# Optimization experiments

Measured on AMD Instinct MI355X. Metric: run time of the kernel, lower is better.

## Reference

```python
import jax, jax.numpy as jnp
import numpy as np

B, C, H, W = 32, 1024, 32, 32  # N = H*W must equal C for the attn_c * attn_s broadcast
C8 = C // 8


def setup_inputs() -> dict:
    key = jax.random.key(0)
    ks = jax.random.split(key, 9)
    s = 1.0 / np.sqrt(C)
    return {
        "z": jax.random.normal(ks[0], (B, C, H, W), jnp.float32),
        "x": jax.random.normal(ks[1], (B, C, H, W), jnp.float32),
        "y": jax.random.normal(ks[2], (B, C, H, W), jnp.float32),
        "Wq": jax.random.normal(ks[3], (C8, C), jnp.float32) * s,
        "bq": jax.random.normal(ks[4], (C8,), jnp.float32) * 0.01,
        "Wk": jax.random.normal(ks[5], (C8, C), jnp.float32) * s,
        "bk": jax.random.normal(ks[6], (C8,), jnp.float32) * 0.01,
        "Wv": jax.random.normal(ks[7], (C, C), jnp.float32) * s,
        "bv": jax.random.normal(ks[8], (C,), jnp.float32) * 0.01,
    }


def reference(z, x, y, Wq, bq, Wk, bk, Wv, bv):
    b, c, h, w = x.shape
    n = h * w
    xf = x.reshape(b, c, n)
    yf = y.reshape(b, c, n)
    zf = z.reshape(b, c, n)

    # 1x1 convs == channel matmuls
    q = jnp.einsum('oc,bcn->bon', Wq, xf) + bq[None, :, None]   # (B, C/8, N)
    k = jnp.einsum('oc,bcn->bon', Wk, yf) + bk[None, :, None]   # (B, C/8, N)

    # channel-projected spatial attention: (B, N, N)
    energy_c = jnp.einsum('bcn,bcm->bnm', q, k)
    attention_c = jax.nn.softmax(energy_c, axis=-1)

    # raw channel attention: (B, C, C)
    energy_s = jnp.einsum('bcn,bdn->bcd', xf, yf)
    energy_s = jnp.max(energy_s, axis=-1, keepdims=True) - energy_s
    attention_s = jax.nn.softmax(energy_s, axis=-1)

    # multiplicative combine + third softmax (requires N == C)
    attention = jax.nn.softmax(attention_c * attention_s, axis=-1)

    v = jnp.einsum('oc,bcn->bon', Wv, zf) + bv[None, :, None]   # (B, C, N)
    # out[b,c,m] = sum_n v[b,c,n] * attention[b,m,n]  (value @ attention^T)
    out = jnp.einsum('bcn,bmn->bcm', v, attention)
    return z + out.reshape(b, c, h, w)
```

## Files before the change

kernel.cpp:

```cpp
#include <hip/hip_runtime.h>
#include <hip/hip_bf16.h>

typedef __attribute__((ext_vector_type(8))) short s8_t;
typedef __attribute__((ext_vector_type(4))) float f4_t;

__device__ __forceinline__ unsigned short f2bf(float f) {
  union { float f; unsigned u; } x; x.f = f;
  unsigned r = x.u + 0x7fffu + ((x.u >> 16) & 1u);
  return (unsigned short)(r >> 16);
}

__device__ __forceinline__ void split2(float e0, float e1, unsigned& hp, unsigned& lp) {
  unsigned b0 = __float_as_uint(e0), b1 = __float_as_uint(e1);
  unsigned h0 = b0 & 0xFFFF0000u, h1 = b1 & 0xFFFF0000u;
  hp = (b0 >> 16) | h1;
  float l0 = e0 - __uint_as_float(h0), l1 = e1 - __uint_as_float(h1);
  lp = (__float_as_uint(l0) >> 16) | (__float_as_uint(l1) & 0xFFFF0000u);
}

__device__ __forceinline__ void gload16(const void* g, void* l) {
  __builtin_amdgcn_global_load_lds(
      (const __attribute__((address_space(1))) void*)g,
      (__attribute__((address_space(3))) void*)l, 16, 0, 0);
}

__device__ __forceinline__ void swz_grid(int& bx, int& by, int& bz) {
  const int gx = gridDim.x, gy = gridDim.y;
  const int nwg = gx * gy * gridDim.z;
  const int flat = (blockIdx.z * gy + blockIdx.y) * gx + blockIdx.x;
  const int s = (flat & 7) * (nwg >> 3) + (flat >> 3);
  bx = s % gx;
  const int r = s / gx;
  by = r % gy;
  bz = r / gy;
}

__global__ __launch_bounds__(256) void k_convert(const float* __restrict__ in,
                                                 unsigned short* __restrict__ out, int n) {
  int i = (blockIdx.x * 256 + threadIdx.x) * 8;
  if (i >= n) return;
  float4 a = *(const float4*)(in + i);
  float4 b = *(const float4*)(in + i + 4);
  ushort4 u0; u0.x = f2bf(a.x); u0.y = f2bf(a.y); u0.z = f2bf(a.z); u0.w = f2bf(a.w);
  ushort4 u1; u1.x = f2bf(b.x); u1.y = f2bf(b.y); u1.z = f2bf(b.z); u1.w = f2bf(b.w);
  *(ushort4*)(out + i) = u0;
  *(ushort4*)(out + i + 4) = u1;
}

__global__ __launch_bounds__(256) void k_transp32(const float* __restrict__ in,
                                                  float* __restrict__ out) {
  __shared__ float tile[64][65];
  const int t = threadIdx.x, b = blockIdx.z;
  const int r0 = blockIdx.y * 64, c0 = blockIdx.x * 64;
  const float* ip = in + (size_t)b * 1048576;
  float* op = out + (size_t)b * 1048576;
  const int tr = t >> 4, tc = (t & 15) * 4;
#pragma unroll
  for (int p = 0; p < 4; ++p) {
    int r = p * 16 + tr;
    float4 v = *(const float4*)(ip + (size_t)(r0 + r) * 1024 + c0 + tc);
    tile[r][tc] = v.x; tile[r][tc + 1] = v.y; tile[r][tc + 2] = v.z; tile[r][tc + 3] = v.w;
  }
  __syncthreads();
#pragma unroll
  for (int p = 0; p < 4; ++p) {
    int n = p * 16 + tr;
    float4 w;
    w.x = tile[tc][n]; w.y = tile[tc + 1][n]; w.z = tile[tc + 2][n]; w.w = tile[tc + 3][n];
    *(float4*)(op + (size_t)(c0 + n) * 1024 + r0 + tc) = w;
  }
}

__global__ __launch_bounds__(256) void k_transpbf(const float* __restrict__ in,
                                                  unsigned short* __restrict__ outt) {
  __shared__ unsigned short tile[64][72];
  const int t = threadIdx.x, b = blockIdx.z;
  const int r0 = blockIdx.y * 64, c0 = blockIdx.x * 64;
  const float* ip = in + (size_t)b * 1048576;
  const int tr = t >> 4, tc = (t & 15) * 4;
#pragma unroll
  for (int p = 0; p < 4; ++p) {
    int r = p * 16 + tr;
    float4 v = *(const float4*)(ip + (size_t)(r0 + r) * 1024 + c0 + tc);
    tile[r][tc] = f2bf(v.x); tile[r][tc + 1] = f2bf(v.y);
    tile[r][tc + 2] = f2bf(v.z); tile[r][tc + 3] = f2bf(v.w);
  }
  __syncthreads();
#pragma unroll
  for (int p = 0; p < 4; ++p) {
    int n = p * 16 + tr;
    ushort4 w;
    w.x = tile[tc][n]; w.y = tile[tc + 1][n]; w.z = tile[tc + 2][n]; w.w = tile[tc + 3][n];
    *(ushort4*)(outt + (size_t)b * 1048576 + (size_t)(c0 + n) * 1024 + r0 + tc) = w;
  }
}

__device__ __forceinline__ void split_write(unsigned short* buf, int wbase,
                                            const float* av, const float* bv) {
  unsigned ah[8], al[8], bh[8], bl[8];
#pragma unroll
  for (int p = 0; p < 8; ++p) {
    split2(av[2 * p], av[2 * p + 1], ah[p], al[p]);
    split2(bv[2 * p], bv[2 * p + 1], bh[p], bl[p]);
  }
  *(uint4*)(buf + wbase) = *(uint4*)(ah);
  *(uint4*)(buf + wbase + 8) = *(uint4*)(ah + 4);
  *(uint4*)(buf + 4096 + wbase) = *(uint4*)(al);
  *(uint4*)(buf + 4096 + wbase + 8) = *(uint4*)(al + 4);
  *(uint4*)(buf + 8192 + wbase) = *(uint4*)(bh);
  *(uint4*)(buf + 8192 + wbase + 8) = *(uint4*)(bh + 4);
  *(uint4*)(buf + 12288 + wbase) = *(uint4*)(bl);
  *(uint4*)(buf + 12288 + wbase + 8) = *(uint4*)(bl + 4);
}

template <int BIAS_MODE>
__global__ __launch_bounds__(256) void k_mfma3(
    const float* __restrict__ A, int lda, long long sA,
    const float* __restrict__ B, int ldb, long long sB,
    float* __restrict__ C, int ldc, long long sC,
    const float* __restrict__ bias, int K) {
  __shared__ __align__(16) unsigned short sm[16384];
  int bxs, bys, bz; swz_grid(bxs, bys, bz);
  const int tid = threadIdx.x;
  const int lane = tid & 63, wave = tid >> 6;
  const int wr = wave >> 1, wc = wave & 1;
  const int m0 = bxs * 128, n0 = bys * 128;

  const int sr = tid >> 1, sh = (tid & 1) * 16;
  const float* ag = A + (long long)bz * sA + (long long)(m0 + sr) * lda + sh;
  const float* bg = B + (long long)bz * sB + (long long)(n0 + sr) * ldb + sh;
  const int wbase = sr * 32 + sh;

  const int lr = lane & 15, lg = lane >> 4;
  const int fa = (wr * 64 + lr) * 32 + lg * 8;
  const int fb = (wc * 64 + lr) * 32 + lg * 8;

  f4_t acc[4][4];
#pragma unroll
  for (int i = 0; i < 4; ++i)
#pragma unroll
    for (int j = 0; j < 4; ++j) acc[i][j] = (f4_t)0.f;

  for (int k0 = 0; k0 < K; k0 += 32) {
    float av[16], bv[16];
#pragma unroll
    for (int p = 0; p < 4; ++p) {
      *(float4*)(av + p * 4) = *(const float4*)(ag + p * 4);
      *(float4*)(bv + p * 4) = *(const float4*)(bg + p * 4);
    }
    split_write(sm, wbase, av, bv);
    ag += 32; bg += 32;
    __syncthreads();
    const unsigned short* Ahp = sm;
    const unsigned short* Alp = sm + 4096;
    const unsigned short* Bhp = sm + 8192;
    const unsigned short* Blp = sm + 12288;
    s8_t fah[4], fbh[4], ftmp[4];
#pragma unroll
    for (int f = 0; f < 4; ++f) {
      fah[f] = *(const s8_t*)(Ahp + fa + f * 512);
      fbh[f] = *(const s8_t*)(Bhp + fb + f * 512);
    }
#pragma unroll
    for (int i = 0; i < 4; ++i)
#pragma unroll
      for (int j = 0; j < 4; ++j)
        acc[i][j] = __builtin_amdgcn_mfma_f32_16x16x32_bf16(fah[i], fbh[j], acc[i][j], 0, 0, 0);
#pragma unroll
    for (int f = 0; f < 4; ++f) ftmp[f] = *(const s8_t*)(Blp + fb + f * 512);
#pragma unroll
    for (int i = 0; i < 4; ++i)
#pragma unroll
      for (int j = 0; j < 4; ++j)
        acc[i][j] = __builtin_amdgcn_mfma_f32_16x16x32_bf16(fah[i], ftmp[j], acc[i][j], 0, 0, 0);
#pragma unroll
    for (int f = 0; f < 4; ++f) ftmp[f] = *(const s8_t*)(Alp + fa + f * 512);
#pragma unroll
    for (int i = 0; i < 4; ++i)
#pragma unroll
      for (int j = 0; j < 4; ++j)
        acc[i][j] = __builtin_amdgcn_mfma_f32_16x16x32_bf16(ftmp[i], fbh[j], acc[i][j], 0, 0, 0);
    __syncthreads();
  }

#pragma unroll
  for (int i = 0; i < 4; ++i) {
    const int rbase = m0 + wr * 64 + i * 16 + lg * 4;
#pragma unroll
    for (int j = 0; j < 4; ++j) {
      const int col = n0 + wc * 64 + j * 16 + lr;
      float bc = (BIAS_MODE == 2) ? bias[col] : 0.f;
#pragma unroll
      for (int e = 0; e < 4; ++e) {
        float v = acc[i][j][e];
        if (BIAS_MODE == 2) v += bc;
        C[(long long)bz * sC + (long long)(rbase + e) * ldc + col] = v;
      }
    }
  }
}

template <int BIAS_MODE, bool OUT_BF16, bool RESID>
__global__ __launch_bounds__(256) void k_mfma(
    const unsigned short* __restrict__ A, int lda, long long sA,
    const unsigned short* __restrict__ B, int ldb, long long sB,
    void* __restrict__ Cp, int ldc, long long sC,
    const float* __restrict__ bias,
    const float* __restrict__ resid, long long sR, int K) {
  __shared__ __align__(16) unsigned short As[12288];
  __shared__ __align__(16) unsigned short Bs[12288];
  int bxs, bys, bz; swz_grid(bxs, bys, bz);
  const int tid = threadIdx.x;
  const int lane = tid & 63, wave = tid >> 6;
  const int wr = wave >> 1, wc = wave & 1;
  const int m0 = bxs * 128, n0 = bys * 128;

  const int ch0 = wave * 64 + lane, ch1 = ch0 + 256;
  const unsigned short* pa0 = A + (long long)bz * sA + (long long)(m0 + (ch0 >> 2)) * lda + (ch0 & 3) * 8;
  const unsigned short* pa1 = A + (long long)bz * sA + (long long)(m0 + (ch1 >> 2)) * lda + (ch1 & 3) * 8;
  const unsigned short* pb0 = B + (long long)bz * sB + (long long)(n0 + (ch0 >> 2)) * ldb + (ch0 & 3) * 8;
  const unsigned short* pb1 = B + (long long)bz * sB + (long long)(n0 + (ch1 >> 2)) * ldb + (ch1 & 3) * 8;

  const int lr = lane & 15, lg = lane >> 4;
  const int fa = (wr * 64 + lr) * 32 + lg * 8;
  const int fb = (wc * 64 + lr) * 32 + lg * 8;

  f4_t acc[4][4];
#pragma unroll
  for (int i = 0; i < 4; ++i)
#pragma unroll
    for (int j = 0; j < 4; ++j) acc[i][j] = (f4_t)0.f;

  char* a0 = (char*)As; char* a1 = a0 + 8192; char* a2 = a0 + 16384;
  char* b0 = (char*)Bs; char* b1 = b0 + 8192; char* b2 = b0 + 16384;

  auto stage = [&](char* la, char* lb) {
    gload16(pa0, la + wave * 1024);
    gload16(pa1, la + 4096 + wave * 1024);
    gload16(pb0, lb + wave * 1024);
    gload16(pb1, lb + 4096 + wave * 1024);
    pa0 += 32; pa1 += 32; pb0 += 32; pb1 += 32;
  };

  const int nt = K >> 5;
  stage(a0, b0);
  stage(a1, b1);

  for (int t = 0; t < nt; ++t) {
    if (t + 2 < nt) {
      stage(a2, b2);
      asm volatile("s_waitcnt vmcnt(8)" ::: "memory");
    } else if (t + 1 < nt) {
      asm volatile("s_waitcnt vmcnt(4)" ::: "memory");
    } else {
      asm volatile("s_waitcnt vmcnt(0)" ::: "memory");
    }
    __builtin_amdgcn_sched_barrier(0);
    __builtin_amdgcn_s_barrier();
    __builtin_amdgcn_sched_barrier(0);
    const unsigned short* ap = (const unsigned short*)a0;
    const unsigned short* bp = (const unsigned short*)b0;
    s8_t af[4], bf[4];
#pragma unroll
    for (int f = 0; f < 4; ++f) {
      af[f] = *(const s8_t*)(ap + fa + f * 512);
      bf[f] = *(const s8_t*)(bp + fb + f * 512);
    }
#pragma unroll
    for (int i = 0; i < 4; ++i)
#pragma unroll
      for (int j = 0; j < 4; ++j)
        acc[i][j] = __builtin_amdgcn_mfma_f32_16x16x32_bf16(af[i], bf[j], acc[i][j], 0, 0, 0);
    __builtin_amdgcn_sched_barrier(0);
    __builtin_amdgcn_s_barrier();
    __builtin_amdgcn_sched_barrier(0);
    char* ta = a0; a0 = a1; a1 = a2; a2 = ta;
    char* tb = b0; b0 = b1; b1 = b2; b2 = tb;
  }

#pragma unroll
  for (int i = 0; i < 4; ++i) {
    const int rbase = m0 + wr * 64 + i * 16 + lg * 4;
#pragma unroll
    for (int j = 0; j < 4; ++j) {
      const int col = n0 + wc * 64 + j * 16 + lr;
#pragma unroll
      for (int e = 0; e < 4; ++e) {
        const int row = rbase + e;
        float v = acc[i][j][e];
        if (BIAS_MODE == 1) v += bias[row];
        const long long off = (long long)bz * sC + (long long)row * ldc + col;
        if (RESID) v += resid[(long long)bz * sR + (long long)row * ldc + col];
        if (OUT_BF16) ((unsigned short*)Cp)[off] = f2bf(v);
        else          ((float*)Cp)[off] = v;
      }
    }
  }
}

__device__ __forceinline__ float wave_red_max(float v) {
#pragma unroll
  for (int o = 32; o > 0; o >>= 1) v = fmaxf(v, __shfl_down(v, o, 64));
  return v;
}
__device__ __forceinline__ float wave_red_sum(float v) {
#pragma unroll
  for (int o = 32; o > 0; o >>= 1) v += __shfl_down(v, o, 64);
  return v;
}
__device__ __forceinline__ float block_red_max(float v, float* red) {
  v = wave_red_max(v);
  if ((threadIdx.x & 63) == 0) red[threadIdx.x >> 6] = v;
  __syncthreads();
  v = fmaxf(fmaxf(red[0], red[1]), fmaxf(red[2], red[3]));
  __syncthreads();
  return v;
}
__device__ __forceinline__ float block_red_sum(float v, float* red) {
  v = wave_red_sum(v);
  if ((threadIdx.x & 63) == 0) red[threadIdx.x >> 6] = v;
  __syncthreads();
  v = red[0] + red[1] + red[2] + red[3];
  __syncthreads();
  return v;
}

__global__ __launch_bounds__(256) void k_combine(float* __restrict__ ec,
                                                 const float* __restrict__ es) {
  __shared__ float red[4];
  const size_t row = blockIdx.x;
  float* cp = ec + row * 1024;
  const float* sp = es + row * 1024;
  const int tid = threadIdx.x;
  float4 c4 = ((const float4*)cp)[tid];
  float4 s4 = ((const float4*)sp)[tid];

  float mx = fmaxf(fmaxf(c4.x, c4.y), fmaxf(c4.z, c4.w));
  mx = block_red_max(mx, red);
  float e0 = __expf(c4.x - mx), e1 = __expf(c4.y - mx);
  float e2 = __expf(c4.z - mx), e3 = __expf(c4.w - mx);
  float sc = block_red_sum(e0 + e1 + e2 + e3, red);

  float t0 = -s4.x, t1 = -s4.y, t2 = -s4.z, t3 = -s4.w;
  float mt = fmaxf(fmaxf(t0, t1), fmaxf(t2, t3));
  mt = block_red_max(mt, red);
  float f0 = __expf(t0 - mt), f1 = __expf(t1 - mt);
  float f2 = __expf(t2 - mt), f3 = __expf(t3 - mt);
  float ss = block_red_sum(f0 + f1 + f2 + f3, red);

  const float rc = 1.f / sc, rs = 1.f / ss;
  float g0 = __expf((e0 * rc) * (f0 * rs));
  float g1 = __expf((e1 * rc) * (f1 * rs));
  float g2 = __expf((e2 * rc) * (f2 * rs));
  float g3 = __expf((e3 * rc) * (f3 * rs));
  float s3 = block_red_sum(g0 + g1 + g2 + g3, red);
  const float r3 = 1.f / s3;
  ushort4 o;
  o.x = f2bf(g0 * r3); o.y = f2bf(g1 * r3); o.z = f2bf(g2 * r3); o.w = f2bf(g3 * r3);
  ((ushort4*)cp)[tid] = o;
}

extern "C" void kernel_launch(void* const* d_in, const int* in_sizes, int n_in,
                              void* d_out, int out_size, void* d_ws, size_t ws_size,
                              hipStream_t stream) {
  const float* z = (const float*)d_in[0];
  const float* x = (const float*)d_in[1];
  const float* y = (const float*)d_in[2];
  const float* Wq = (const float*)d_in[3];
  const float* bq = (const float*)d_in[4];
  const float* Wk = (const float*)d_in[5];
  const float* bk = (const float*)d_in[6];
  const float* Wv = (const float*)d_in[7];
  const float* bv = (const float*)d_in[8];
  float* out = (float*)d_out;

  char* ws = (char*)d_ws;
  float* es = (float*)ws;
  unsigned short* z_t = (unsigned short*)ws;
  unsigned short* v_bf = z_t + 33554432;
  char* wsB = ws + 134217728;
  float* xytf = (float*)wsB;
  float* ec = (float*)wsB;
  unsigned short* attn = (unsigned short*)wsB;
  char* wsC = ws + 268435456;
  float* q_t = (float*)wsC;
  float* k_t = q_t + 4194304;
  unsigned short* wv = (unsigned short*)wsC;

  dim3 blk(256);
  hipLaunchKernelGGL(k_transp32, dim3(16, 16, 32), blk, 0, stream, x, xytf);
  hipLaunchKernelGGL((k_mfma3<2>), dim3(8, 1, 32), blk, 0, stream,
                     xytf, 1024, 1048576LL, Wq, 1024, 0LL, q_t, 128, 131072LL, bq, 1024);
  hipLaunchKernelGGL(k_transp32, dim3(16, 16, 32), blk, 0, stream, y, xytf);
  hipLaunchKernelGGL((k_mfma3<2>), dim3(8, 1, 32), blk, 0, stream,
                     xytf, 1024, 1048576LL, Wk, 1024, 0LL, k_t, 128, 131072LL, bk, 1024);
  hipLaunchKernelGGL((k_mfma3<0>), dim3(8, 8, 32), blk, 0, stream,
                     x, 1024, 1048576LL, y, 1024, 1048576LL, es, 1024, 1048576LL,
                     (const float*)nullptr, 1024);
  hipLaunchKernelGGL((k_mfma3<0>), dim3(8, 8, 32), blk, 0, stream,
                     q_t, 128, 131072LL, k_t, 128, 131072LL, ec, 1024, 1048576LL,
                     (const float*)nullptr, 128);
  hipLaunchKernelGGL(k_combine, dim3(32768), blk, 0, stream, ec, es);
  hipLaunchKernelGGL(k_transpbf, dim3(16, 16, 32), blk, 0, stream, z, z_t);
  hipLaunchKernelGGL(k_convert, dim3(512), blk, 0, stream, Wv, wv, 1048576);
  hipLaunchKernelGGL((k_mfma<1, true, false>), dim3(8, 8, 32), blk, 0, stream,
                     wv, 1024, 0LL, z_t, 1024, 1048576LL, (void*)v_bf, 1024, 1048576LL,
                     bv, (const float*)nullptr, 0LL, 1024);
  hipLaunchKernelGGL((k_mfma<0, false, true>), dim3(8, 8, 32), blk, 0, stream,
                     v_bf, 1024, 1048576LL, attn, 2048, 2097152LL, (void*)out, 1024, 1048576LL,
                     (const float*)nullptr, z, 1048576LL, 1024);
}
```

Measured before the change: 866.2 us.

## Fuse Q/K projections into split-bf16 MFMA kernel and enlarge bf16 GEMM tiles

```diff
diff --git a/kernel.cpp b/kernel.cpp
--- a/kernel.cpp
+++ b/kernel.cpp
@@ -8,6 +8,14 @@
   union { float f; unsigned u; } x; x.f = f;
   unsigned r = x.u + 0x7fffu + ((x.u >> 16) & 1u);
   return (unsigned short)(r >> 16);
+}
+
+__device__ __forceinline__ void split1(float v, unsigned short& h, unsigned short& l) {
+  unsigned b = __float_as_uint(v);
+  unsigned hb = b & 0xFFFF0000u;
+  h = (unsigned short)(b >> 16);
+  float lo = v - __uint_as_float(hb);
+  l = (unsigned short)(__float_as_uint(lo) >> 16);
 }
 
 __device__ __forceinline__ void split2(float e0, float e1, unsigned& hp, unsigned& lp) {
@@ -47,13 +55,14 @@
   *(ushort4*)(out + i + 4) = u1;
 }
 
-__global__ __launch_bounds__(256) void k_transp32(const float* __restrict__ in,
-                                                  float* __restrict__ out) {
+__global__ __launch_bounds__(256) void k_tsplitT(const float* __restrict__ in,
+                                                 unsigned short* __restrict__ th,
+                                                 unsigned short* __restrict__ tl) {
   __shared__ float tile[64][65];
-  const int t = threadIdx.x, b = blockIdx.z;
+  const int t = threadIdx.x, bz = blockIdx.z;
   const int r0 = blockIdx.y * 64, c0 = blockIdx.x * 64;
-  const float* ip = in + (size_t)b * 1048576;
-  float* op = out + (size_t)b * 1048576;
+  const float* ip = in + (size_t)bz * 1048576;
+  const size_t ob = (size_t)bz * 1048576;
   const int tr = t >> 4, tc = (t & 15) * 4;
 #pragma unroll
   for (int p = 0; p < 4; ++p) {
@@ -65,9 +74,11 @@
 #pragma unroll
   for (int p = 0; p < 4; ++p) {
     int n = p * 16 + tr;
-    float4 w;
-    w.x = tile[tc][n]; w.y = tile[tc + 1][n]; w.z = tile[tc + 2][n]; w.w = tile[tc + 3][n];
-    *(float4*)(op + (size_t)(c0 + n) * 1024 + r0 + tc) = w;
+    float a = tile[tc][n], b = tile[tc + 1][n], c = tile[tc + 2][n], d = tile[tc + 3][n];
+    ushort4 h, l;
+    split1(a, h.x, l.x); split1(b, h.y, l.y); split1(c, h.z, l.z); split1(d, h.w, l.w);
+    *(ushort4*)(th + ob + (size_t)(c0 + n) * 1024 + r0 + tc) = h;
+    *(ushort4*)(tl + ob + (size_t)(c0 + n) * 1024 + r0 + tc) = l;
   }
 }
 
@@ -200,45 +211,144 @@
   }
 }
 
+__global__ __launch_bounds__(256) void k_qk3p(
+    const unsigned short* __restrict__ Axh, const unsigned short* __restrict__ Axl,
+    const unsigned short* __restrict__ Ayh, const unsigned short* __restrict__ Ayl,
+    const float* __restrict__ Wqf, const float* __restrict__ Wkf,
+    const float* __restrict__ bqf, const float* __restrict__ bkf,
+    float* __restrict__ Qt, float* __restrict__ Kt) {
+  __shared__ __align__(16) unsigned short smAh[4096], smAl[4096], smBh[4096], smBl[4096];
+  int bx, by, bz; swz_grid(bx, by, bz);
+  const unsigned short* Ah = by ? Ayh : Axh;
+  const unsigned short* Al = by ? Ayl : Axl;
+  const float* Bf = by ? Wkf : Wqf;
+  const float* bias = by ? bkf : bqf;
+  float* Of = by ? Kt : Qt;
+
+  const int tid = threadIdx.x, lane = tid & 63, wave = tid >> 6;
+  const int wr = wave >> 1, wc = wave & 1;
+  const int m0 = bx * 128;
+
+  const int ch0 = wave * 64 + lane, ch1 = ch0 + 256;
+  const int r0 = ch0 >> 2, kc0 = (ch0 & 3) * 8, r1 = ch1 >> 2, kc1 = (ch1 & 3) * 8;
+  const unsigned short* pah0 = Ah + (long long)bz * 1048576 + (long long)(m0 + r0) * 1024 + kc0;
+  const unsigned short* pah1 = Ah + (long long)bz * 1048576 + (long long)(m0 + r1) * 1024 + kc1;
+  const unsigned short* pal0 = Al + (long long)bz * 1048576 + (long long)(m0 + r0) * 1024 + kc0;
+  const unsigned short* pal1 = Al + (long long)bz * 1048576 + (long long)(m0 + r1) * 1024 + kc1;
+  char* dAh0 = (char*)smAh + wave * 1024; char* dAh1 = dAh0 + 4096;
+  char* dAl0 = (char*)smAl + wave * 1024; char* dAl1 = dAl0 + 4096;
+
+  const int sr = tid >> 1, sh = (tid & 1) * 16;
+  const float* bg = Bf + (long long)sr * 1024 + sh;
+  const int wbase = sr * 32 + sh;
+
+  const int lr = lane & 15, lg = lane >> 4;
+  const int fa = (wr * 64 + lr) * 32 + lg * 8;
+  const int fb = (wc * 64 + lr) * 32 + lg * 8;
+
+  f4_t acc[4][4];
+#pragma unroll
+  for (int i = 0; i < 4; ++i)
+#pragma unroll
+    for (int j = 0; j < 4; ++j) acc[i][j] = (f4_t)0.f;
+
+  for (int k0 = 0; k0 < 1024; k0 += 32) {
+    gload16(pah0, dAh0); gload16(pah1, dAh1);
+    gload16(pal0, dAl0); gload16(pal1, dAl1);
+    pah0 += 32; pah1 += 32; pal0 += 32; pal1 += 32;
+    float bv[16];
+#pragma unroll
+    for (int p = 0; p < 4; ++p) *(float4*)(bv + p * 4) = *(const float4*)(bg + p * 4);
+    bg += 32;
+    unsigned bh[8], bl[8];
+#pragma unroll
+    for (int p = 0; p < 8; ++p) split2(bv[2 * p], bv[2 * p + 1], bh[p], bl[p]);
+    *(uint4*)(smBh + wbase) = *(uint4*)(bh);
+    *(uint4*)(smBh + wbase + 8) = *(uint4*)(bh + 4);
+    *(uint4*)(smBl + wbase) = *(uint4*)(bl);
+    *(uint4*)(smBl + wbase + 8) = *(uint4*)(bl + 4);
+    __syncthreads();
+    s8_t fah[4], fbh[4], ft[4];
+#pragma unroll
+    for (int f = 0; f < 4; ++f) {
+      fah[f] = *(const s8_t*)(smAh + fa + f * 512);
+      fbh[f] = *(const s8_t*)(smBh + fb + f * 512);
+    }
+#pragma unroll
+    for (int i = 0; i < 4; ++i)
+#pragma unroll
+      for (int j = 0; j < 4; ++j)
+        acc[i][j] = __builtin_amdgcn_mfma_f32_16x16x32_bf16(fah[i], fbh[j], acc[i][j], 0, 0, 0);
+#pragma unroll
+    for (int f = 0; f < 4; ++f) ft[f] = *(const s8_t*)(smBl + fb + f * 512);
+#pragma unroll
+    for (int i = 0; i < 4; ++i)
+#pragma unroll
+      for (int j = 0; j < 4; ++j)
+        acc[i][j] = __builtin_amdgcn_mfma_f32_16x16x32_bf16(fah[i], ft[j], acc[i][j], 0, 0, 0);
+#pragma unroll
+    for (int f = 0; f < 4; ++f) ft[f] = *(const s8_t*)(smAl + fa + f * 512);
+#pragma unroll
+    for (int i = 0; i < 4; ++i)
+#pragma unroll
+      for (int j = 0; j < 4; ++j)
+        acc[i][j] = __builtin_amdgcn_mfma_f32_16x16x32_bf16(ft[i], fbh[j], acc[i][j], 0, 0, 0);
+    __syncthreads();
+  }
+
+#pragma unroll
+  for (int i = 0; i < 4; ++i) {
+    const int rbase = m0 + wr * 64 + i * 16 + lg * 4;
+#pragma unroll
+    for (int j = 0; j < 4; ++j) {
+      const int col = wc * 64 + j * 16 + lr;
+      const float bc = bias[col];
+#pragma unroll
+      for (int e = 0; e < 4; ++e)
+        Of[(long long)bz * 131072 + (long long)(rbase + e) * 128 + col] = acc[i][j][e] + bc;
+    }
+  }
+}
+
 template <int BIAS_MODE, bool OUT_BF16, bool RESID>
-__global__ __launch_bounds__(256) void k_mfma(
+__global__ __launch_bounds__(512) void k_mfma256(
     const unsigned short* __restrict__ A, int lda, long long sA,
     const unsigned short* __restrict__ B, int ldb, long long sB,
     void* __restrict__ Cp, int ldc, long long sC,
     const float* __restrict__ bias,
     const float* __restrict__ resid, long long sR, int K) {
-  __shared__ __align__(16) unsigned short As[12288];
-  __shared__ __align__(16) unsigned short Bs[12288];
+  __shared__ __align__(16) unsigned short As[24576];
+  __shared__ __align__(16) unsigned short Bs[24576];
   int bxs, bys, bz; swz_grid(bxs, bys, bz);
   const int tid = threadIdx.x;
   const int lane = tid & 63, wave = tid >> 6;
-  const int wr = wave >> 1, wc = wave & 1;
-  const int m0 = bxs * 128, n0 = bys * 128;
-
-  const int ch0 = wave * 64 + lane, ch1 = ch0 + 256;
-  const unsigned short* pa0 = A + (long long)bz * sA + (long long)(m0 + (ch0 >> 2)) * lda + (ch0 & 3) * 8;
-  const unsigned short* pa1 = A + (long long)bz * sA + (long long)(m0 + (ch1 >> 2)) * lda + (ch1 & 3) * 8;
-  const unsigned short* pb0 = B + (long long)bz * sB + (long long)(n0 + (ch0 >> 2)) * ldb + (ch0 & 3) * 8;
-  const unsigned short* pb1 = B + (long long)bz * sB + (long long)(n0 + (ch1 >> 2)) * ldb + (ch1 & 3) * 8;
+  const int wr = wave >> 2, wc = wave & 3;
+  const int m0 = bxs * 256, n0 = bys * 256;
+
+  const int cA0 = tid, cA1 = tid + 512;
+  const unsigned short* pa0 = A + (long long)bz * sA + (long long)(m0 + (cA0 >> 2)) * lda + (cA0 & 3) * 8;
+  const unsigned short* pa1 = A + (long long)bz * sA + (long long)(m0 + (cA1 >> 2)) * lda + (cA1 & 3) * 8;
+  const unsigned short* pb0 = B + (long long)bz * sB + (long long)(n0 + (cA0 >> 2)) * ldb + (cA0 & 3) * 8;
+  const unsigned short* pb1 = B + (long long)bz * sB + (long long)(n0 + (cA1 >> 2)) * ldb + (cA1 & 3) * 8;
 
   const int lr = lane & 15, lg = lane >> 4;
-  const int fa = (wr * 64 + lr) * 32 + lg * 8;
+  const int fa = (wr * 128 + lr) * 32 + lg * 8;
   const int fb = (wc * 64 + lr) * 32 + lg * 8;
 
-  f4_t acc[4][4];
-#pragma unroll
-  for (int i = 0; i < 4; ++i)
+  f4_t acc[8][4];
+#pragma unroll
+  for (int i = 0; i < 8; ++i)
 #pragma unroll
     for (int j = 0; j < 4; ++j) acc[i][j] = (f4_t)0.f;
 
-  char* a0 = (char*)As; char* a1 = a0 + 8192; char* a2 = a0 + 16384;
-  char* b0 = (char*)Bs; char* b1 = b0 + 8192; char* b2 = b0 + 16384;
-
-  auto stage = [&](char* la, char* lb) {
-    gload16(pa0, la + wave * 1024);
-    gload16(pa1, la + 4096 + wave * 1024);
-    gload16(pb0, lb + wave * 1024);
-    gload16(pb1, lb + 4096 + wave * 1024);
+  unsigned short* a0 = As; unsigned short* a1 = As + 8192; unsigned short* a2 = As + 16384;
+  unsigned short* b0 = Bs; unsigned short* b1 = Bs + 8192; unsigned short* b2 = Bs + 16384;
+
+  auto stage = [&](unsigned short* la, unsigned short* lb) {
+    gload16(pa0, (char*)la + wave * 1024);
+    gload16(pa1, (char*)la + 8192 + wave * 1024);
+    gload16(pb0, (char*)lb + wave * 1024);
+    gload16(pb1, (char*)lb + 8192 + wave * 1024);
     pa0 += 32; pa1 += 32; pb0 += 32; pb1 += 32;
   };
 
@@ -258,29 +368,28 @@
     __builtin_amdgcn_sched_barrier(0);
     __builtin_amdgcn_s_barrier();
     __builtin_amdgcn_sched_barrier(0);
-    const unsigned short* ap = (const unsigned short*)a0;
-    const unsigned short* bp = (const unsigned short*)b0;
-    s8_t af[4], bf[4];
-#pragma unroll
-    for (int f = 0; f < 4; ++f) {
-      af[f] = *(const s8_t*)(ap + fa + f * 512);
-      bf[f] = *(const s8_t*)(bp + fb + f * 512);
-    }
-#pragma unroll
-    for (int i = 0; i < 4; ++i)
+    const unsigned short* ap = a0;
+    const unsigned short* bp = b0;
+    s8_t af[8], bf[4];
+#pragma unroll
+    for (int i = 0; i < 8; ++i) af[i] = *(const s8_t*)(ap + fa + i * 512);
+#pragma unroll
+    for (int j = 0; j < 4; ++j) bf[j] = *(const s8_t*)(bp + fb + j * 512);
+#pragma unroll
+    for (int i = 0; i < 8; ++i)
 #pragma unroll
       for (int j = 0; j < 4; ++j)
         acc[i][j] = __builtin_amdgcn_mfma_f32_16x16x32_bf16(af[i], bf[j], acc[i][j], 0, 0, 0);
     __builtin_amdgcn_sched_barrier(0);
     __builtin_amdgcn_s_barrier();
     __builtin_amdgcn_sched_barrier(0);
-    char* ta = a0; a0 = a1; a1 = a2; a2 = ta;
-    char* tb = b0; b0 = b1; b1 = b2; b2 = tb;
-  }
-
-#pragma unroll
-  for (int i = 0; i < 4; ++i) {
-    const int rbase = m0 + wr * 64 + i * 16 + lg * 4;
+    unsigned short* ta = a0; a0 = a1; a1 = a2; a2 = ta;
+    unsigned short* tb = b0; b0 = b1; b1 = b2; b2 = tb;
+  }
+
+#pragma unroll
+  for (int i = 0; i < 8; ++i) {
+    const int rbase = m0 + wr * 128 + i * 16 + lg * 4;
 #pragma unroll
     for (int j = 0; j < 4; ++j) {
       const int col = n0 + wc * 64 + j * 16 + lr;
@@ -375,11 +484,14 @@
   float* out = (float*)d_out;
 
   char* ws = (char*)d_ws;
+  unsigned short* yth = (unsigned short*)ws;
+  unsigned short* ytl = yth + 33554432;
   float* es = (float*)ws;
   unsigned short* z_t = (unsigned short*)ws;
   unsigned short* v_bf = z_t + 33554432;
   char* wsB = ws + 134217728;
-  float* xytf = (float*)wsB;
+  unsigned short* xth = (unsigned short*)wsB;
+  unsigned short* xtl = xth + 33554432;
   float* ec = (float*)wsB;
   unsigned short* attn = (unsigned short*)wsB;
   char* wsC = ws + 268435456;
@@ -388,12 +500,10 @@
   unsigned short* wv = (unsigned short*)wsC;
 
   dim3 blk(256);
-  hipLaunchKernelGGL(k_transp32, dim3(16, 16, 32), blk, 0, stream, x, xytf);
-  hipLaunchKernelGGL((k_mfma3<2>), dim3(8, 1, 32), blk, 0, stream,
-                     xytf, 1024, 1048576LL, Wq, 1024, 0LL, q_t, 128, 131072LL, bq, 1024);
-  hipLaunchKernelGGL(k_transp32, dim3(16, 16, 32), blk, 0, stream, y, xytf);
-  hipLaunchKernelGGL((k_mfma3<2>), dim3(8, 1, 32), blk, 0, stream,
-                     xytf, 1024, 1048576LL, Wk, 1024, 0LL, k_t, 128, 131072LL, bk, 1024);
+  hipLaunchKernelGGL(k_tsplitT, dim3(16, 16, 32), blk, 0, stream, x, xth, xtl);
+  hipLaunchKernelGGL(k_tsplitT, dim3(16, 16, 32), blk, 0, stream, y, yth, ytl);
+  hipLaunchKernelGGL(k_qk3p, dim3(8, 2, 32), blk, 0, stream,
+                     xth, xtl, yth, ytl, Wq, Wk, bq, bk, q_t, k_t);
   hipLaunchKernelGGL((k_mfma3<0>), dim3(8, 8, 32), blk, 0, stream,
                      x, 1024, 1048576LL, y, 1024, 1048576LL, es, 1024, 1048576LL,
                      (const float*)nullptr, 1024);
@@ -403,10 +513,10 @@
   hipLaunchKernelGGL(k_combine, dim3(32768), blk, 0, stream, ec, es);
   hipLaunchKernelGGL(k_transpbf, dim3(16, 16, 32), blk, 0, stream, z, z_t);
   hipLaunchKernelGGL(k_convert, dim3(512), blk, 0, stream, Wv, wv, 1048576);
-  hipLaunchKernelGGL((k_mfma<1, true, false>), dim3(8, 8, 32), blk, 0, stream,
+  hipLaunchKernelGGL((k_mfma256<1, true, false>), dim3(4, 4, 32), dim3(512), 0, stream,
                      wv, 1024, 0LL, z_t, 1024, 1048576LL, (void*)v_bf, 1024, 1048576LL,
                      bv, (const float*)nullptr, 0LL, 1024);
-  hipLaunchKernelGGL((k_mfma<0, false, true>), dim3(8, 8, 32), blk, 0, stream,
+  hipLaunchKernelGGL((k_mfma256<0, false, true>), dim3(4, 4, 32), dim3(512), 0, stream,
                      v_bf, 1024, 1048576LL, attn, 2048, 2097152LL, (void*)out, 1024, 1048576LL,
                      (const float*)nullptr, z, 1048576LL, 1024);
 }
```

New measurement: 796.6 us. 1.09x faster.
